# Kernel tuning notes

Hardware: AMD Instinct MI355X
Metric: run time of the kernel (lower is better)

## Reference

```python
import jax, jax.numpy as jnp
import numpy as np

B, S, D = 2, 2048, 1024
H, KV, HD = 16, 4, 64          # heads, kv heads, head_dim = D//H
I, E, K = 3584, 4, 2            # ffn intermediate, routed experts, top_k
WIN = 512                       # sliding window
EPS = 1e-5
THETA = 1000000.0
LIMIT = 7.0                     # swiglu clamp
NREP = H // KV
NEG = -1e30

def _rms(x, w):
    return x * jax.lax.rsqrt(jnp.mean(x * x, axis=-1, keepdims=True) + EPS) * w

def _rot_half(x):
    h = x.shape[-1] // 2
    return jnp.concatenate([-x[..., h:], x[..., :h]], axis=-1)

def _ffn(x, gw, uw, dw):
    g = jnp.minimum(x @ gw.T, LIMIT)
    u = jnp.clip(x @ uw.T, -LIMIT, LIMIT)
    return (jax.nn.silu(g) * u) @ dw.T

def setup_inputs():
    key = jax.random.key(0)
    ks = jax.random.split(key, 16)
    # rotary embeddings [S, HD]
    inv = 1.0 / (THETA ** (jnp.arange(0, HD, 2, dtype=jnp.float32) / HD))
    freqs = jnp.outer(jnp.arange(S, dtype=jnp.float32), inv)
    emb = jnp.concatenate([freqs, freqs], axis=-1)
    s = 0.02
    return dict(
        x=jax.random.normal(ks[0], (B, S, D), jnp.float32),
        cos=jnp.cos(emb), sin=jnp.sin(emb),
        attn_norm_w=jnp.ones((D,), jnp.float32),
        post_norm_w=jnp.ones((D,), jnp.float32),
        q_norm_w=jnp.ones((HD,), jnp.float32),
        k_norm_w=jnp.ones((HD,), jnp.float32),
        wq=jax.random.normal(ks[1], (H * HD, D), jnp.float32) * s,
        wk=jax.random.normal(ks[2], (KV * HD, D), jnp.float32) * s,
        wv=jax.random.normal(ks[3], (KV * HD, D), jnp.float32) * s,
        wo=jax.random.normal(ks[4], (D, H * HD), jnp.float32) * s,
        sinks=jax.random.normal(ks[5], (H,), jnp.float32),
        gate_w=jax.random.normal(ks[6], (E, D), jnp.float32) * s,
        eg_w=jax.random.normal(ks[7], (E, I, D), jnp.float32) * s,
        eu_w=jax.random.normal(ks[8], (E, I, D), jnp.float32) * s,
        ed_w=jax.random.normal(ks[9], (E, D, I), jnp.float32) * s,
        sg_w=jax.random.normal(ks[10], (I, D), jnp.float32) * s,
        su_w=jax.random.normal(ks[11], (I, D), jnp.float32) * s,
        sd_w=jax.random.normal(ks[12], (D, I), jnp.float32) * s,
    )

def _forward(x, cos, sin, attn_norm_w, wq, wk, wv, wo, q_norm_w, k_norm_w,
             sinks, post_norm_w, gate_w, eg_w, eu_w, ed_w, sg_w, su_w, sd_w):
    # ---- attention sublayer ----
    hin = _rms(x, attn_norm_w)
    q = (hin @ wq.T).reshape(B, S, H, HD)
    k = (hin @ wk.T).reshape(B, S, KV, HD)
    v = (hin @ wv.T).reshape(B, S, KV, HD)
    q = _rms(q, q_norm_w)
    k = _rms(k, k_norm_w)
    c, sn = cos[None, :, None, :], sin[None, :, None, :]
    q = q * c + _rot_half(q) * sn
    k = k * c + _rot_half(k) * sn
    k = jnp.repeat(k, NREP, axis=2)  # GQA -> [B,S,H,HD]
    v = jnp.repeat(v, NREP, axis=2)
    scores = jnp.einsum('bihd,bjhd->bhij', q, k) / np.sqrt(HD).astype(np.float32)
    idx = jnp.arange(S)
    allowed = (idx[:, None] >= idx[None, :]) & (idx[None, :] > idx[:, None] - WIN)
    scores = jnp.where(allowed[None, None], scores, NEG)
    sink = jnp.broadcast_to(sinks.reshape(1, H, 1, 1), (B, H, S, 1))
    ext = jnp.concatenate([scores, sink], axis=-1)           # [B,H,S,S+1]
    w = jax.nn.softmax(ext.astype(jnp.float32), axis=-1)[..., :-1].astype(x.dtype)
    attn = jnp.einsum('bhij,bjhd->bihd', w, v).reshape(B, S, H * HD) @ wo.T
    h1 = x + attn
    # ---- MoE FFN sublayer ----
    m = _rms(h1, post_norm_w).reshape(-1, D)                 # [T,D]
    T = m.shape[0]
    gs = jax.nn.softmax(m @ gate_w.T, axis=-1)               # [T,E]
    tw, ti = jax.lax.top_k(gs, K)
    tw = tw / (jnp.sum(tw, axis=-1, keepdims=True) + 1e-20)  # norm_topk_prob
    wd = jnp.zeros((T, E), m.dtype).at[jnp.arange(T)[:, None], ti].add(tw)
    g = jnp.minimum(jnp.einsum('td,eid->tei', m, eg_w), LIMIT)
    u = jnp.clip(jnp.einsum('td,eid->tei', m, eu_w), -LIMIT, LIMIT)
    eo = jnp.einsum('tei,edi->ted', jax.nn.silu(g) * u, ed_w)
    y = jnp.einsum('ted,te->td', eo, wd) + _ffn(m, sg_w, su_w, sd_w)
    return h1 + y.reshape(B, S, D)

def reference(x, cos, sin, attn_norm_w, post_norm_w, q_norm_w, k_norm_w,
              wq, wk, wv, wo, sinks, gate_w, eg_w, eu_w, ed_w, sg_w, su_w, sd_w):
    return _forward(x, cos, sin, attn_norm_w, wq, wk, wv, wo, q_norm_w, k_norm_w,
                    sinks, post_norm_w, gate_w, eg_w, eu_w, ed_w, sg_w, su_w, sd_w)
```

## Files before the change

kernel.cpp:

```cpp
#include <hip/hip_runtime.h>
#include <cstdint>
#include <cstddef>

#define S_LEN 2048
#define BATCH 2
#define DMODEL 1024
#define NH 16
#define NKV 4
#define HDIM 64
#define NTOK 4096
#define IDIM 3584
#define NEXP 4
#define WINSZ 512
#define EPSV 1e-5f
#define LIMV 7.0f
#define CATMAX 13056

typedef unsigned short u16;
typedef unsigned int u32;
typedef __bf16 bf16x8 __attribute__((ext_vector_type(8)));
typedef float f32x4 __attribute__((ext_vector_type(4)));
typedef u32 u32x4 __attribute__((ext_vector_type(4)));
typedef u16 u16x4 __attribute__((ext_vector_type(4)));

__device__ __forceinline__ u16 f2b(float f) {
  union { float f; u32 u; } v; v.f = f;
  return (u16)((v.u + 0x7fffu + ((v.u >> 16) & 1u)) >> 16);
}
__device__ __forceinline__ float b2f(u16 h) {
  union { u32 u; float f; } v; v.u = ((u32)h) << 16; return v.f;
}
__device__ __forceinline__ float wave_sum(float x) {
#pragma unroll
  for (int o = 32; o > 0; o >>= 1) x += __shfl_xor(x, o);
  return x;
}
__device__ __forceinline__ void gld16(const void* g, void* l) {
  __builtin_amdgcn_global_load_lds(
      (const __attribute__((address_space(1))) u32*)g,
      (__attribute__((address_space(3))) u32*)l, 16, 0, 0);
}

__global__ void k_init(int* cnt) {
  if (threadIdx.x < NEXP) cnt[threadIdx.x] = 0;
}

struct CvtArgs {
  const float* src[10];
  u16* dh[10];
  u16* dl[10];
  int n4[10];
};
__global__ __launch_bounds__(256) void k_convert(CvtArgs a) {
  int ai = blockIdx.y;
  const f32x4* s = (const f32x4*)a.src[ai];
  u16* dh = a.dh[ai];
  u16* dl = a.dl[ai];
  int n4 = a.n4[ai];
  for (int i = blockIdx.x * 256 + threadIdx.x; i < n4; i += gridDim.x * 256) {
    f32x4 v = s[i];
    u16x4 h;
    h.x = f2b(v.x); h.y = f2b(v.y); h.z = f2b(v.z); h.w = f2b(v.w);
    ((u16x4*)dh)[i] = h;
    if (dl) {
      u16x4 lo;
      lo.x = f2b(v.x - b2f(h.x)); lo.y = f2b(v.y - b2f(h.y));
      lo.z = f2b(v.z - b2f(h.z)); lo.w = f2b(v.w - b2f(h.w));
      ((u16x4*)dl)[i] = lo;
    }
  }
}

__global__ __launch_bounds__(256) void k_rms_split(const float* __restrict__ x,
                                                   const float* __restrict__ w,
                                                   u16* __restrict__ oh, u16* __restrict__ ol) {
  int row = blockIdx.x;
  int t = threadIdx.x;
  const f32x4* xr = (const f32x4*)(x + (size_t)row * DMODEL);
  f32x4 v = xr[t];
  float ss = v.x * v.x + v.y * v.y + v.z * v.z + v.w * v.w;
  ss = wave_sum(ss);
  __shared__ float red[4];
  int wid = t >> 6;
  if ((t & 63) == 0) red[wid] = ss;
  __syncthreads();
  float tot = red[0] + red[1] + red[2] + red[3];
  float r = rsqrtf(tot * (1.0f / DMODEL) + EPSV);
  f32x4 wv = ((const f32x4*)w)[t];
  float y0 = v.x * r * wv.x, y1 = v.y * r * wv.y, y2 = v.z * r * wv.z, y3 = v.w * r * wv.w;
  u16x4 h; h.x = f2b(y0); h.y = f2b(y1); h.z = f2b(y2); h.w = f2b(y3);
  u16x4 lo; lo.x = f2b(y0 - b2f(h.x)); lo.y = f2b(y1 - b2f(h.y));
  lo.z = f2b(y2 - b2f(h.z)); lo.w = f2b(y3 - b2f(h.w));
  ((u16x4*)(oh + (size_t)row * DMODEL))[t] = h;
  ((u16x4*)(ol + (size_t)row * DMODEL))[t] = lo;
}

__global__ __launch_bounds__(256) void k_qkprep(const float* __restrict__ qkv,
                                                const float* __restrict__ cosb,
                                                const float* __restrict__ sinb,
                                                const float* __restrict__ qw,
                                                const float* __restrict__ kw,
                                                u16* __restrict__ qhh, u16* __restrict__ qll,
                                                u16* __restrict__ khh, u16* __restrict__ kll,
                                                u16* __restrict__ vhh, u16* __restrict__ vll) {
  int t = blockIdx.x;
  int b = t / S_LEN, s = t - b * S_LEN;
  int wid = threadIdx.x >> 6, l = threadIdx.x & 63;
  const float* row = qkv + (size_t)t * 1536;
  float c = cosb[s * 64 + l], sn = sinb[s * 64 + l];
#pragma unroll
  for (int ii = 0; ii < 6; ii++) {
    int u = wid + 4 * ii;
    if (u < 16) {
      float v = row[u * 64 + l];
      float ss = wave_sum(v * v);
      float r = rsqrtf(ss * (1.0f / 64.0f) + EPSV);
      float vn = v * r * qw[l];
      float p = __shfl_xor(vn, 32);
      float o = (l < 32) ? (vn * c - p * sn) : (vn * c + p * sn);
      o *= 0.125f;
      size_t base = (((size_t)(b * NH + u)) * S_LEN + s) * 64 + l;
      u16 hi = f2b(o);
      qhh[base] = hi; qll[base] = f2b(o - b2f(hi));
    } else if (u < 20) {
      int kv = u - 16;
      float v = row[1024 + kv * 64 + l];
      float ss = wave_sum(v * v);
      float r = rsqrtf(ss * (1.0f / 64.0f) + EPSV);
      float vn = v * r * kw[l];
      float p = __shfl_xor(vn, 32);
      float o = (l < 32) ? (vn * c - p * sn) : (vn * c + p * sn);
      size_t base = (((size_t)(b * NKV + kv)) * S_LEN + s) * 64 + l;
      u16 hi = f2b(o);
      khh[base] = hi; kll[base] = f2b(o - b2f(hi));
    } else {
      int kv = u - 20;
      float v = row[1280 + kv * 64 + l];
      size_t base = (((size_t)(b * NKV + kv)) * S_LEN + s) * 64 + l;
      u16 hi = f2b(v);
      vhh[base] = hi; vll[base] = f2b(v - b2f(hi));
    }
  }
}

__global__ __launch_bounds__(256) void k_vtrans(const u16* __restrict__ vh,
                                                const u16* __restrict__ vl,
                                                u16* __restrict__ vth, u16* __restrict__ vtl) {
  int kb = blockIdx.x;
  int gg = blockIdx.y;
  __shared__ u16 Th[128 * 64], Tl[128 * 64];
  int t = threadIdx.x;
  const u16* sh = vh + (((size_t)gg * S_LEN) + kb * 128) * 64;
  const u16* sl = vl + (((size_t)gg * S_LEN) + kb * 128) * 64;
#pragma unroll
  for (int p = 0; p < 8; p++) {
    int idx = p * 256 + t;
    int key = idx >> 4, dq = idx & 15;
    u16x4 a = *(const u16x4*)(sh + key * 64 + dq * 4);
    u16x4 bb = *(const u16x4*)(sl + key * 64 + dq * 4);
    int off = key * 128 + ((dq * 8) ^ ((key & 7) << 4));
    *(u16x4*)((char*)Th + off) = a;
    *(u16x4*)((char*)Tl + off) = bb;
  }
  __syncthreads();
  int d = t >> 2, kq = t & 3;
  u16 outh[32], outl[32];
#pragma unroll
  for (int jj = 0; jj < 32; jj++) {
    int key = kq * 32 + jj;
    int off = key * 128 + ((d * 2) ^ ((key & 7) << 4));
    outh[jj] = *(const u16*)((const char*)Th + off);
    outl[jj] = *(const u16*)((const char*)Tl + off);
  }
  u16* dsth = vth + (((size_t)gg * 64) + d) * S_LEN + kb * 128 + kq * 32;
  u16* dstl = vtl + (((size_t)gg * 64) + d) * S_LEN + kb * 128 + kq * 32;
#pragma unroll
  for (int q4 = 0; q4 < 8; q4++) {
    u16x4 a = {outh[q4 * 4], outh[q4 * 4 + 1], outh[q4 * 4 + 2], outh[q4 * 4 + 3]};
    u16x4 bb = {outl[q4 * 4], outl[q4 * 4 + 1], outl[q4 * 4 + 2], outl[q4 * 4 + 3]};
    *(u16x4*)(dsth + q4 * 4) = a;
    *(u16x4*)(dstl + q4 * 4) = bb;
  }
}

__global__ __launch_bounds__(256) void k_attn_mfma(
    const u16* __restrict__ qhp, const u16* __restrict__ qlp,
    const u16* __restrict__ khp, const u16* __restrict__ klp,
    const u16* __restrict__ vthp, const u16* __restrict__ vtlp,
    const float* __restrict__ sinks,
    u16* __restrict__ oh, u16* __restrict__ ol) {
  int qt = blockIdx.x;
  int bh = blockIdx.y;
  int h = bh & 15, b = bh >> 4;
  int kvg = b * NKV + (h >> 2);
  int qbase = qt * 64;
  int t = threadIdx.x, w = t >> 6, l = t & 63;
  int g = l >> 4, li = l & 15;

  __shared__ u16 Qh[4096], Ql[4096], Kh[4096], Kl[4096], Vh[4096], Vl[4096];
  __shared__ u16 Ph[4][1024], Pl[4][1024];

  {
    const u16* sh = qhp + (((size_t)bh * S_LEN) + qbase) * 64;
    const u16* sl = qlp + (((size_t)bh * S_LEN) + qbase) * 64;
#pragma unroll
    for (int p = 0; p < 2; p++) {
      int idx = p * 256 + t;
      int row = idx >> 3, seg = idx & 7;
      u32x4 a = *(const u32x4*)(sh + row * 64 + seg * 8);
      u32x4 bb = *(const u32x4*)(sl + row * 64 + seg * 8);
      int off = row * 128 + ((seg * 16) ^ ((row & 7) << 4));
      *(u32x4*)((char*)Qh + off) = a;
      *(u32x4*)((char*)Ql + off) = bb;
    }
  }

  float m_[4], lsum[4];
  f32x4 accv[4];
  float sk = sinks[h];
#pragma unroll
  for (int j = 0; j < 4; j++) { m_[j] = sk; lsum[j] = 1.0f; }
#pragma unroll
  for (int nt = 0; nt < 4; nt++) accv[nt] = (f32x4){0.f, 0.f, 0.f, 0.f};

  int j0s = qbase - WINSZ; if (j0s < 0) j0s = 0;
  const u16* khb = khp + ((size_t)kvg * S_LEN) * 64;
  const u16* klb = klp + ((size_t)kvg * S_LEN) * 64;
  const u16* vthb = vthp + ((size_t)kvg * 64) * S_LEN;
  const u16* vtlb = vtlp + ((size_t)kvg * 64) * S_LEN;

  for (int j0 = j0s; j0 <= qbase; j0 += 64) {
    __syncthreads();
#pragma unroll
    for (int p = 0; p < 2; p++) {
      int idx = p * 256 + t;
      int row = idx >> 3, seg = idx & 7;
      int off = row * 128 + ((seg * 16) ^ ((row & 7) << 4));
      *(u32x4*)((char*)Kh + off) = *(const u32x4*)(khb + ((size_t)(j0 + row)) * 64 + seg * 8);
      *(u32x4*)((char*)Kl + off) = *(const u32x4*)(klb + ((size_t)(j0 + row)) * 64 + seg * 8);
      *(u32x4*)((char*)Vh + off) = *(const u32x4*)(vthb + (size_t)row * S_LEN + j0 + seg * 8);
      *(u32x4*)((char*)Vl + off) = *(const u32x4*)(vtlb + (size_t)row * S_LEN + j0 + seg * 8);
    }
    __syncthreads();

    f32x4 S[4];
#pragma unroll
    for (int nt = 0; nt < 4; nt++) S[nt] = (f32x4){0.f, 0.f, 0.f, 0.f};
#pragma unroll
    for (int ks = 0; ks < 2; ks++) {
      int arow = w * 16 + li;
      int coff = ks * 64 + g * 16;
      int ao = arow * 128 + (coff ^ ((arow & 7) << 4));
      bf16x8 qah = *(const bf16x8*)((char*)Qh + ao);
      bf16x8 qal = *(const bf16x8*)((char*)Ql + ao);
#pragma unroll
      for (int nt = 0; nt < 4; nt++) {
        int brow = nt * 16 + li;
        int bo = brow * 128 + (coff ^ ((brow & 7) << 4));
        bf16x8 kbh = *(const bf16x8*)((char*)Kh + bo);
        bf16x8 kbl = *(const bf16x8*)((char*)Kl + bo);
        S[nt] = __builtin_amdgcn_mfma_f32_16x16x32_bf16(qah, kbh, S[nt], 0, 0, 0);
        S[nt] = __builtin_amdgcn_mfma_f32_16x16x32_bf16(qah, kbl, S[nt], 0, 0, 0);
        S[nt] = __builtin_amdgcn_mfma_f32_16x16x32_bf16(qal, kbh, S[nt], 0, 0, 0);
      }
    }

    float scj[4];
#pragma unroll
    for (int j = 0; j < 4; j++) {
      int q = qbase + w * 16 + g * 4 + j;
      float sv[4];
      float mx = -1e30f;
#pragma unroll
      for (int nt = 0; nt < 4; nt++) {
        int key = j0 + nt * 16 + li;
        bool ok = (key <= q) && (key > q - WINSZ);
        sv[nt] = ok ? S[nt][j] : -1e30f;
        mx = fmaxf(mx, sv[nt]);
      }
#pragma unroll
      for (int o = 1; o < 16; o <<= 1) mx = fmaxf(mx, __shfl_xor(mx, o));
      float mn = fmaxf(m_[j], mx);
      float sc = __expf(m_[j] - mn);
      float ps = 0.f;
      float pv[4];
#pragma unroll
      for (int nt = 0; nt < 4; nt++) { pv[nt] = __expf(sv[nt] - mn); ps += pv[nt]; }
#pragma unroll
      for (int o = 1; o < 16; o <<= 1) ps += __shfl_xor(ps, o);
      lsum[j] = lsum[j] * sc + ps;
      m_[j] = mn;
      scj[j] = sc;
      int prow = g * 4 + j;
#pragma unroll
      for (int nt = 0; nt < 4; nt++) {
        int pb = prow * 128 + ((nt * 32 + li * 2) ^ ((prow & 7) << 4));
        u16 hi = f2b(pv[nt]);
        *(u16*)((char*)Ph[w] + pb) = hi;
        *(u16*)((char*)Pl[w] + pb) = f2b(pv[nt] - b2f(hi));
      }
    }
#pragma unroll
    for (int nt = 0; nt < 4; nt++) {
      f32x4 a = accv[nt];
      a[0] *= scj[0]; a[1] *= scj[1]; a[2] *= scj[2]; a[3] *= scj[3];
      accv[nt] = a;
    }

#pragma unroll
    for (int ks = 0; ks < 2; ks++) {
      int coff = ks * 64 + g * 16;
      int pb = li * 128 + (coff ^ ((li & 7) << 4));
      bf16x8 pah = *(const bf16x8*)((char*)Ph[w] + pb);
      bf16x8 pal = *(const bf16x8*)((char*)Pl[w] + pb);
#pragma unroll
      for (int nt = 0; nt < 4; nt++) {
        int vrow = nt * 16 + li;
        int vo = vrow * 128 + (coff ^ ((vrow & 7) << 4));
        bf16x8 vbh = *(const bf16x8*)((char*)Vh + vo);
        bf16x8 vbl = *(const bf16x8*)((char*)Vl + vo);
        accv[nt] = __builtin_amdgcn_mfma_f32_16x16x32_bf16(pah, vbh, accv[nt], 0, 0, 0);
        accv[nt] = __builtin_amdgcn_mfma_f32_16x16x32_bf16(pah, vbl, accv[nt], 0, 0, 0);
        accv[nt] = __builtin_amdgcn_mfma_f32_16x16x32_bf16(pal, vbh, accv[nt], 0, 0, 0);
      }
    }
  }

  float inv[4];
#pragma unroll
  for (int j = 0; j < 4; j++) inv[j] = 1.0f / lsum[j];
#pragma unroll
  for (int nt = 0; nt < 4; nt++) {
#pragma unroll
    for (int j = 0; j < 4; j++) {
      float o = accv[nt][j] * inv[j];
      int token = b * S_LEN + qbase + w * 16 + g * 4 + j;
      size_t off = (size_t)token * (NH * HDIM) + h * 64 + nt * 16 + li;
      u16 hi = f2b(o);
      oh[off] = hi;
      ol[off] = f2b(o - b2f(hi));
    }
  }
}

__global__ __launch_bounds__(256) void k_routing1(const float* __restrict__ h1,
                                                  const float* __restrict__ pw,
                                                  const float* __restrict__ gw,
                                                  u16* __restrict__ mb,
                                                  float* __restrict__ lgbuf) {
  int row = blockIdx.x;
  int t = threadIdx.x;
  int wid = t >> 6;
  const f32x4* xr = (const f32x4*)(h1 + (size_t)row * DMODEL);
  f32x4 v = xr[t];
  float ss = wave_sum(v.x * v.x + v.y * v.y + v.z * v.z + v.w * v.w);
  __shared__ float red[4];
  __shared__ float redp[4][4];
  if ((t & 63) == 0) red[wid] = ss;
  __syncthreads();
  float tot = red[0] + red[1] + red[2] + red[3];
  float r = rsqrtf(tot * (1.0f / DMODEL) + EPSV);
  f32x4 w4 = ((const f32x4*)pw)[t];
  float m0 = v.x * r * w4.x, m1 = v.y * r * w4.y, m2 = v.z * r * w4.z, m3 = v.w * r * w4.w;
  u16x4 hb; hb.x = f2b(m0); hb.y = f2b(m1); hb.z = f2b(m2); hb.w = f2b(m3);
  ((u16x4*)(mb + (size_t)row * DMODEL))[t] = hb;
#pragma unroll
  for (int e = 0; e < NEXP; e++) {
    f32x4 g4 = ((const f32x4*)(gw + (size_t)e * DMODEL))[t];
    float pe = wave_sum(m0 * g4.x + m1 * g4.y + m2 * g4.z + m3 * g4.w);
    if ((t & 63) == 0) redp[wid][e] = pe;
  }
  __syncthreads();
  if (t < NEXP) {
    float lg = redp[0][t] + redp[1][t] + redp[2][t] + redp[3][t];
    lgbuf[(size_t)row * NEXP + t] = lg;
  }
}

__global__ __launch_bounds__(256) void k_route2(const float* __restrict__ lgbuf,
                                                float* __restrict__ wd,
                                                int* __restrict__ cnt,
                                                int* __restrict__ idxb) {
  __shared__ int lcnt[NEXP], gbase[NEXP];
  int t = threadIdx.x;
  int token = blockIdx.x * 256 + t;
  if (t < NEXP) lcnt[t] = 0;
  __syncthreads();
  f32x4 lgv = ((const f32x4*)lgbuf)[token];
  float lg[4] = {lgv.x, lgv.y, lgv.z, lgv.w};
  int i1 = 0;
#pragma unroll
  for (int e = 1; e < NEXP; e++) if (lg[e] > lg[i1]) i1 = e;
  int i2 = -1;
#pragma unroll
  for (int e = 0; e < NEXP; e++) if (e != i1 && (i2 < 0 || lg[e] > lg[i2])) i2 = e;
  float d = __expf(lg[i2] - lg[i1]);
  float w1 = 1.0f / (1.0f + d);
  float w2 = 1.0f - w1;
  float wrow[4] = {0.f, 0.f, 0.f, 0.f};
  wrow[i1] = w1; wrow[i2] = w2;
  ((f32x4*)wd)[token] = (f32x4){wrow[0], wrow[1], wrow[2], wrow[3]};
  int r1 = atomicAdd(&lcnt[i1], 1);
  int r2 = atomicAdd(&lcnt[i2], 1);
  __syncthreads();
  if (t < NEXP) gbase[t] = atomicAdd(&cnt[t], lcnt[t]);
  __syncthreads();
  idxb[i1 * NTOK + gbase[i1] + r1] = token * 2;
  idxb[i2 * NTOK + gbase[i2] + r2] = token * 2 + 1;
}

__global__ __launch_bounds__(256) void k_route3(const int* __restrict__ cnt,
                                                const int* __restrict__ idxb,
                                                const float* __restrict__ wd,
                                                int* __restrict__ idxcat,
                                                float* __restrict__ wcat,
                                                int* __restrict__ pref) {
  int i = blockIdx.x * 256 + threadIdx.x;
  int c0 = cnt[0], c1 = cnt[1], c2 = cnt[2], c3 = cnt[3];
  int p1 = (c0 + 255) & ~255;
  int p2 = p1 + ((c1 + 255) & ~255);
  int p3 = p2 + ((c2 + 255) & ~255);
  int p4 = p3 + ((c3 + 255) & ~255);
  int p5 = p4 + NTOK;
  if (i == 0) {
    pref[0] = 0; pref[1] = p1; pref[2] = p2; pref[3] = p3; pref[4] = p4; pref[5] = p5;
  }
  if (i >= CATMAX) return;
  if (i >= p5) { idxcat[i] = -1; wcat[i] = 0.f; return; }
  if (i >= p4) {
    idxcat[i] = (i - p4) * 4 + 2;
    wcat[i] = 1.0f;
    return;
  }
  int e, base, cn;
  if (i < p1) { e = 0; base = 0; cn = c0; }
  else if (i < p2) { e = 1; base = p1; cn = c1; }
  else if (i < p3) { e = 2; base = p2; cn = c2; }
  else { e = 3; base = p3; cn = c3; }
  int j = i - base;
  if (j < cn) {
    int entry = idxb[e * NTOK + j];
    idxcat[i] = (entry >> 1) * 4 + (entry & 1);
    wcat[i] = wd[(size_t)(entry >> 1) * NEXP + e];
  } else {
    idxcat[i] = -1;
    wcat[i] = 0.f;
  }
}

template <bool DUAL>
__global__ __launch_bounds__(512, 2) void k256(
    const u16* __restrict__ A, const u16* __restrict__ B1e,
    const u16* __restrict__ B2e,
    int lda, int ldb, int K,
    const int* __restrict__ idxcat, const float* __restrict__ wcat,
    const int* __restrict__ pref,
    u16* __restrict__ actout, u16* __restrict__ y3) {
  __shared__ u16 As[2][256 * 64];
  __shared__ u16 Bs[2][128 * 64];
  __shared__ u16 Bus[2][DUAL ? 128 * 64 : 1];
  int tm = blockIdx.y, tn = blockIdx.x;
  int Meff = pref[5];
  int r0 = tm * 256;
  if (r0 >= Meff) return;
  int e = (r0 < pref[1]) ? 0 : (r0 < pref[2]) ? 1 : (r0 < pref[3]) ? 2
          : (r0 < pref[4]) ? 3 : 4;
  const u16* B1 = B1e + (size_t)e * IDIM * DMODEL;
  const u16* B2 = DUAL ? (B2e + (size_t)e * IDIM * DMODEL) : nullptr;

  int t = threadIdx.x;
  int w = t >> 6, l = t & 63;
  int wm = w >> 2, wn = w & 3;
  int li = l & 15, lh = l >> 4;

  size_t aOff[4];
  int seg = t & 7;
#pragma unroll
  for (int c = 0; c < 4; c++) {
    int r = c * 64 + (t >> 3);
    int swz = (seg ^ (r & 7)) * 8;
    int row;
    if constexpr (DUAL) {
      int en = idxcat[r0 + r];
      row = (en >= 0) ? (en >> 2) : 0;
    } else {
      row = r0 + r;
    }
    aOff[c] = (size_t)row * lda + swz;
  }
  size_t bOff[2];
#pragma unroll
  for (int c = 0; c < 2; c++) {
    int r = c * 64 + (t >> 3);
    int swz = (seg ^ (r & 7)) * 8;
    bOff[c] = (size_t)(tn * 128 + r) * ldb + swz;
  }
  int wlds = w * 1024;

  f32x4 acc[8][2];
  f32x4 accU[DUAL ? 8 : 1][2];
#pragma unroll
  for (int f = 0; f < 8; f++)
#pragma unroll
    for (int cf = 0; cf < 2; cf++) {
      acc[f][cf] = (f32x4){0.f, 0.f, 0.f, 0.f};
      if constexpr (DUAL) accU[f][cf] = (f32x4){0.f, 0.f, 0.f, 0.f};
    }

  auto stage = [&](int buf, int k0) {
    char* ab = (char*)As[buf];
#pragma unroll
    for (int c = 0; c < 4; c++) gld16(A + aOff[c] + k0, ab + c * 8192 + wlds);
    char* bb = (char*)Bs[buf];
#pragma unroll
    for (int c = 0; c < 2; c++) gld16(B1 + bOff[c] + k0, bb + c * 8192 + wlds);
    if constexpr (DUAL) {
      char* ub = (char*)Bus[buf];
#pragma unroll
      for (int c = 0; c < 2; c++) gld16(B2 + bOff[c] + k0, ub + c * 8192 + wlds);
    }
  };

  stage(0, 0);
  __syncthreads();

  int NT = K >> 6;
  int cur = 0;
  for (int kt = 0; kt < NT; kt++) {
    if (kt + 1 < NT) stage(cur ^ 1, (kt + 1) << 6);
#pragma unroll
    for (int kk = 0; kk < 2; kk++) {
      bf16x8 af[8];
#pragma unroll
      for (int f = 0; f < 8; f++) {
        int r = wm * 128 + f * 16 + li;
        af[f] = *(const bf16x8*)((const char*)As[cur] + r * 128 +
                                 (((kk * 4 + lh) ^ (r & 7)) << 4));
      }
      bf16x8 bfr[2];
#pragma unroll
      for (int cf = 0; cf < 2; cf++) {
        int r = wn * 32 + cf * 16 + li;
        bfr[cf] = *(const bf16x8*)((const char*)Bs[cur] + r * 128 +
                                   (((kk * 4 + lh) ^ (r & 7)) << 4));
      }
#pragma unroll
      for (int f = 0; f < 8; f++)
#pragma unroll
        for (int cf = 0; cf < 2; cf++)
          acc[f][cf] = __builtin_amdgcn_mfma_f32_16x16x32_bf16(af[f], bfr[cf], acc[f][cf], 0, 0, 0);
      if constexpr (DUAL) {
        bf16x8 bu[2];
#pragma unroll
        for (int cf = 0; cf < 2; cf++) {
          int r = wn * 32 + cf * 16 + li;
          bu[cf] = *(const bf16x8*)((const char*)Bus[cur] + r * 128 +
                                    (((kk * 4 + lh) ^ (r & 7)) << 4));
        }
#pragma unroll
        for (int f = 0; f < 8; f++)
#pragma unroll
          for (int cf = 0; cf < 2; cf++)
            accU[f][cf] = __builtin_amdgcn_mfma_f32_16x16x32_bf16(af[f], bu[cf], accU[f][cf], 0, 0, 0);
      }
    }
    __syncthreads();
    cur ^= 1;
  }

#pragma unroll
  for (int f = 0; f < 8; f++) {
#pragma unroll
    for (int j = 0; j < 4; j++) {
      int r = r0 + wm * 128 + f * 16 + lh * 4 + j;
#pragma unroll
      for (int cf = 0; cf < 2; cf++) {
        int c = tn * 128 + wn * 32 + cf * 16 + li;
        if constexpr (DUAL) {
          float g = acc[f][cf][j];
          float u = accU[f][cf][j];
          float gm = fminf(g, LIMV);
          float um = fminf(fmaxf(u, -LIMV), LIMV);
          float a = gm / (1.0f + __expf(-gm)) * um;
          actout[(size_t)r * IDIM + c] = f2b(a);
        } else {
          int entry = idxcat[r];
          if (entry >= 0) {
            int tok = entry >> 2, slot = entry & 3;
            y3[((size_t)slot * NTOK + tok) * DMODEL + c] = f2b(wcat[r] * acc[f][cf][j]);
          }
        }
      }
    }
  }
}

constexpr int EPI_STORE = 0;
constexpr int EPI_H1 = 1;

template <int EPI>
__global__ __launch_bounds__(256, 2) void k_gemm(
    const u16* __restrict__ Ah, const u16* __restrict__ Al,
    const u16* __restrict__ Bh, const u16* __restrict__ Bl,
    int M, int N, int K, int lda, int ldb,
    float* __restrict__ outF, int ldc, int col0,
    const float* __restrict__ addsrc) {
  __shared__ u16 As[2 * 128 * 32];
  __shared__ u16 Bs[2 * 128 * 32];
  int tm = blockIdx.y, tn = blockIdx.x;
  int t = threadIdx.x;
  int w = t >> 6, l = t & 63;
  int wr = w >> 1, wc = w & 1;

  size_t a0 = (size_t)(tm * 128 + (t >> 2)) * lda + (t & 3) * 8;
  size_t a1 = a0 + (size_t)64 * lda;
  size_t b0 = (size_t)(tn * 128 + (t >> 2)) * ldb + (t & 3) * 8;
  size_t b1 = b0 + (size_t)64 * ldb;

  char* AsW0 = (char*)As + w * 1024;
  char* AsW1 = (char*)As + 4096 + w * 1024;
  char* BsW0 = (char*)Bs + w * 1024;
  char* BsW1 = (char*)Bs + 4096 + w * 1024;

  f32x4 acc[4][4];
#pragma unroll
  for (int i = 0; i < 4; i++)
#pragma unroll
    for (int j = 0; j < 4; j++) acc[i][j] = (f32x4){0.f, 0.f, 0.f, 0.f};

  int arow = wr * 64 + (l & 15);
  int brow = wc * 64 + (l & 15);
  int koff = (l >> 4) * 8;

  for (int k0 = 0; k0 < K; k0 += 32) {
    __syncthreads();
    gld16(Ah + a0 + k0, AsW0);
    gld16(Ah + a1 + k0, AsW1);
    gld16(Bh + b0 + k0, BsW0);
    gld16(Bh + b1 + k0, BsW1);
    gld16(Al + a0 + k0, AsW0 + 8192);
    gld16(Al + a1 + k0, AsW1 + 8192);
    gld16(Bl + b0 + k0, BsW0 + 8192);
    gld16(Bl + b1 + k0, BsW1 + 8192);
    __syncthreads();
    bf16x8 af[2][4], bf[2][4];
#pragma unroll
    for (int mm = 0; mm < 4; mm++) {
      af[0][mm] = *(const bf16x8*)&As[(arow + mm * 16) * 32 + koff];
      bf[0][mm] = *(const bf16x8*)&Bs[(brow + mm * 16) * 32 + koff];
      af[1][mm] = *(const bf16x8*)&As[128 * 32 + (arow + mm * 16) * 32 + koff];
      bf[1][mm] = *(const bf16x8*)&Bs[128 * 32 + (brow + mm * 16) * 32 + koff];
    }
#pragma unroll
    for (int mi = 0; mi < 4; mi++)
#pragma unroll
      for (int ni = 0; ni < 4; ni++) {
        acc[mi][ni] = __builtin_amdgcn_mfma_f32_16x16x32_bf16(af[0][mi], bf[0][ni], acc[mi][ni], 0, 0, 0);
        acc[mi][ni] = __builtin_amdgcn_mfma_f32_16x16x32_bf16(af[0][mi], bf[1][ni], acc[mi][ni], 0, 0, 0);
        acc[mi][ni] = __builtin_amdgcn_mfma_f32_16x16x32_bf16(af[1][mi], bf[0][ni], acc[mi][ni], 0, 0, 0);
      }
  }

  int rb = tm * 128 + wr * 64 + ((l >> 4) << 2);
  int cb = tn * 128 + wc * 64 + (l & 15);
#pragma unroll
  for (int mi = 0; mi < 4; mi++) {
#pragma unroll
    for (int j = 0; j < 4; j++) {
      int r = rb + mi * 16 + j;
#pragma unroll
      for (int ni = 0; ni < 4; ni++) {
        int c = cb + ni * 16;
        float v = acc[mi][ni][j];
        if constexpr (EPI == EPI_STORE) {
          outF[(size_t)r * ldc + col0 + c] = v;
        } else {
          size_t o = (size_t)r * ldc + c;
          outF[o] = v + addsrc[o];
        }
      }
    }
  }
}

__global__ __launch_bounds__(256) void k_final(const float* __restrict__ h1,
                                               const u16* __restrict__ y3,
                                               float* __restrict__ out) {
  int i = blockIdx.x * 256 + threadIdx.x;
  f32x4 a = ((const f32x4*)h1)[i];
  u16x4 s0 = ((const u16x4*)y3)[i];
  u16x4 s1 = ((const u16x4*)(y3 + (size_t)NTOK * DMODEL))[i];
  u16x4 s2 = ((const u16x4*)(y3 + (size_t)2 * NTOK * DMODEL))[i];
  f32x4 r = {a.x + b2f(s0.x) + b2f(s1.x) + b2f(s2.x),
             a.y + b2f(s0.y) + b2f(s1.y) + b2f(s2.y),
             a.z + b2f(s0.z) + b2f(s1.z) + b2f(s2.z),
             a.w + b2f(s0.w) + b2f(s1.w) + b2f(s2.w)};
  ((f32x4*)out)[i] = r;
}

extern "C" void kernel_launch(void* const* d_in, const int* in_sizes, int n_in,
                              void* d_out, int out_size, void* d_ws, size_t ws_size,
                              hipStream_t stream) {
  (void)in_sizes; (void)n_in; (void)out_size; (void)ws_size;
  const float* x = (const float*)d_in[0];
  const float* cosb = (const float*)d_in[1];
  const float* sinb = (const float*)d_in[2];
  const float* anw = (const float*)d_in[3];
  const float* pnw = (const float*)d_in[4];
  const float* qnw = (const float*)d_in[5];
  const float* knw = (const float*)d_in[6];
  const float* wq = (const float*)d_in[7];
  const float* wk = (const float*)d_in[8];
  const float* wv = (const float*)d_in[9];
  const float* wo = (const float*)d_in[10];
  const float* sinks = (const float*)d_in[11];
  const float* gw = (const float*)d_in[12];
  const float* egw = (const float*)d_in[13];
  const float* euw = (const float*)d_in[14];
  const float* edw = (const float*)d_in[15];
  const float* sgw = (const float*)d_in[16];
  const float* suw = (const float*)d_in[17];
  const float* sdw = (const float*)d_in[18];
  float* out = (float*)d_out;

  char* ws = (char*)d_ws;
  size_t off = 0;
  auto alloc = [&](size_t bytes) -> char* {
    char* p = ws + off;
    off += (bytes + 255) & ~(size_t)255;
    return p;
  };
  const size_t EW = (size_t)IDIM * DMODEL;
  u16* wqkvh = (u16*)alloc((size_t)1536 * 1024 * 2);
  u16* wqkvl = (u16*)alloc((size_t)1536 * 1024 * 2);
  u16* woh = (u16*)alloc(1048576 * 2); u16* wol = (u16*)alloc(1048576 * 2);
  u16* egb5 = (u16*)alloc(5 * EW * 2);
  u16* eub5 = (u16*)alloc(5 * EW * 2);
  u16* edb5 = (u16*)alloc(5 * EW * 2);
  float* h1 = (float*)alloc((size_t)NTOK * DMODEL * 4);
  u16* mb = (u16*)alloc((size_t)NTOK * DMODEL * 2);
  u16* y3 = (u16*)alloc((size_t)3 * NTOK * DMODEL * 2);
  float* wdbuf = (float*)alloc((size_t)NTOK * NEXP * 4);
  float* lgbuf = (float*)alloc((size_t)NTOK * NEXP * 4);
  int* cnt = (int*)alloc(256);
  int* idxb = (int*)alloc((size_t)NEXP * NTOK * 4);
  int* idxcat = (int*)alloc((size_t)CATMAX * 4);
  float* wcat = (float*)alloc((size_t)CATMAX * 4);
  int* pref = (int*)alloc(256);
  char* regA = alloc((size_t)CATMAX * IDIM * 2);
  float* qkvb = (float*)regA;
  u16* qh_ = (u16*)(regA + 25165824);
  u16* ql_ = (u16*)(regA + 33554432);
  u16* kh_ = (u16*)(regA + 41943040);
  u16* kl_ = (u16*)(regA + 44040192);
  u16* vh_ = (u16*)(regA + 46137344);
  u16* vl_ = (u16*)(regA + 48234496);
  u16* vth_ = (u16*)(regA + 50331648);
  u16* vtl_ = (u16*)(regA + 52428800);
  u16* hinh = (u16*)(regA + 54525952);
  u16* hinl = (u16*)(regA + 62914560);
  u16* attnh = (u16*)(regA + 71303168);
  u16* attnl = (u16*)(regA + 79691776);
  u16* actcat = (u16*)regA;

  k_init<<<1, 64, 0, stream>>>(cnt);

  CvtArgs ca;
  const float* srcs[10] = {wq, wk, wv, wo, egw, euw, edw, sgw, suw, sdw};
  u16* dhs[10] = {wqkvh, wqkvh + 1048576, wqkvh + 1310720, woh,
                  egb5, eub5, edb5, egb5 + 4 * EW, eub5 + 4 * EW, edb5 + 4 * EW};
  u16* dls[10] = {wqkvl, wqkvl + 1048576, wqkvl + 1310720, wol,
                  nullptr, nullptr, nullptr, nullptr, nullptr, nullptr};
  int ns[10] = {1048576, 262144, 262144, 1048576, 14680064, 14680064, 14680064,
                3670016, 3670016, 3670016};
  for (int i = 0; i < 10; i++) {
    ca.src[i] = srcs[i]; ca.dh[i] = dhs[i]; ca.dl[i] = dls[i]; ca.n4[i] = ns[i] / 4;
  }
  k_convert<<<dim3(2048, 10), 256, 0, stream>>>(ca);

  k_rms_split<<<NTOK, 256, 0, stream>>>(x, anw, hinh, hinl);

  k_gemm<EPI_STORE><<<dim3(12, 32), 256, 0, stream>>>(
      hinh, hinl, wqkvh, wqkvl, NTOK, 1536, 1024, 1024, 1024,
      qkvb, 1536, 0, nullptr);

  k_qkprep<<<NTOK, 256, 0, stream>>>(qkvb, cosb, sinb, qnw, knw,
                                     qh_, ql_, kh_, kl_, vh_, vl_);
  k_vtrans<<<dim3(16, 8), 256, 0, stream>>>(vh_, vl_, vth_, vtl_);
  k_attn_mfma<<<dim3(32, 32), 256, 0, stream>>>(qh_, ql_, kh_, kl_, vth_, vtl_,
                                                sinks, attnh, attnl);

  k_gemm<EPI_H1><<<dim3(8, 32), 256, 0, stream>>>(
      attnh, attnl, woh, wol, NTOK, 1024, 1024, 1024, 1024,
      h1, 1024, 0, x);

  k_routing1<<<NTOK, 256, 0, stream>>>(h1, pnw, gw, mb, lgbuf);
  k_route2<<<16, 256, 0, stream>>>(lgbuf, wdbuf, cnt, idxb);
  k_route3<<<CATMAX / 256, 256, 0, stream>>>(cnt, idxb, wdbuf, idxcat, wcat, pref);

  k256<true><<<dim3(IDIM / 128, CATMAX / 256), 512, 0, stream>>>(
      mb, egb5, eub5, DMODEL, DMODEL, DMODEL, idxcat, wcat, pref, actcat, nullptr);
  k256<false><<<dim3(DMODEL / 128, CATMAX / 256), 512, 0, stream>>>(
      actcat, edb5, nullptr, IDIM, IDIM, IDIM, idxcat, wcat, pref, nullptr, y3);

  k_final<<<4096, 256, 0, stream>>>(h1, y3, out);
}
```

Baseline: 688.9 us.

## Split MoE GEMM into gate-up and down kernels with XCD-aware block swizzle

Splits the templated MoE GEMM into two dedicated kernels. Both remap block IDs so that neighbouring tiles land on the same XCD, which should improve L2 reuse of expert weights. The down-projection kernel now uses a 32-wide K tile with a new LDS layout and launch bounds of 4 blocks per CU, aiming for higher occupancy and less LDS per block. The trade-off is more K iterations and more barriers in the down projection, plus heavier index arithmetic to address the new layout.

```diff
diff --git a/kernel.cpp b/kernel.cpp
--- a/kernel.cpp
+++ b/kernel.cpp
@@ -39,6 +39,11 @@
   __builtin_amdgcn_global_load_lds(
       (const __attribute__((address_space(1))) u32*)g,
       (__attribute__((address_space(3))) u32*)l, 16, 0, 0);
+}
+__device__ __forceinline__ int xcd_swz(int id, int nwg) {
+  int q = nwg >> 3, rr = nwg & 7;
+  int xcd = id & 7, j = id >> 3;
+  return (xcd < rr ? xcd * (q + 1) : rr * (q + 1) + (xcd - rr) * q) + j;
 }
 
 __global__ void k_init(int* cnt) {
@@ -448,25 +453,24 @@
   }
 }
 
-template <bool DUAL>
-__global__ __launch_bounds__(512, 2) void k256(
+__global__ __launch_bounds__(512, 2) void k256gu(
     const u16* __restrict__ A, const u16* __restrict__ B1e,
     const u16* __restrict__ B2e,
-    int lda, int ldb, int K,
-    const int* __restrict__ idxcat, const float* __restrict__ wcat,
-    const int* __restrict__ pref,
-    u16* __restrict__ actout, u16* __restrict__ y3) {
+    const int* __restrict__ idxcat, const int* __restrict__ pref,
+    u16* __restrict__ actout) {
   __shared__ u16 As[2][256 * 64];
   __shared__ u16 Bs[2][128 * 64];
-  __shared__ u16 Bus[2][DUAL ? 128 * 64 : 1];
-  int tm = blockIdx.y, tn = blockIdx.x;
+  __shared__ u16 Bus[2][128 * 64];
+  int nwg = gridDim.x * gridDim.y;
+  int swzid = xcd_swz(blockIdx.y * gridDim.x + blockIdx.x, nwg);
+  int tn = swzid % gridDim.x, tm = swzid / gridDim.x;
   int Meff = pref[5];
   int r0 = tm * 256;
   if (r0 >= Meff) return;
   int e = (r0 < pref[1]) ? 0 : (r0 < pref[2]) ? 1 : (r0 < pref[3]) ? 2
           : (r0 < pref[4]) ? 3 : 4;
   const u16* B1 = B1e + (size_t)e * IDIM * DMODEL;
-  const u16* B2 = DUAL ? (B2e + (size_t)e * IDIM * DMODEL) : nullptr;
+  const u16* B2 = B2e + (size_t)e * IDIM * DMODEL;
 
   int t = threadIdx.x;
   int w = t >> 6, l = t & 63;
@@ -479,32 +483,26 @@
   for (int c = 0; c < 4; c++) {
     int r = c * 64 + (t >> 3);
     int swz = (seg ^ (r & 7)) * 8;
-    int row;
-    if constexpr (DUAL) {
-      int en = idxcat[r0 + r];
-      row = (en >= 0) ? (en >> 2) : 0;
-    } else {
-      row = r0 + r;
-    }
-    aOff[c] = (size_t)row * lda + swz;
+    int en = idxcat[r0 + r];
+    int row = (en >= 0) ? (en >> 2) : 0;
+    aOff[c] = (size_t)row * DMODEL + swz;
   }
   size_t bOff[2];
 #pragma unroll
   for (int c = 0; c < 2; c++) {
     int r = c * 64 + (t >> 3);
     int swz = (seg ^ (r & 7)) * 8;
-    bOff[c] = (size_t)(tn * 128 + r) * ldb + swz;
+    bOff[c] = (size_t)(tn * 128 + r) * DMODEL + swz;
   }
   int wlds = w * 1024;
 
-  f32x4 acc[8][2];
-  f32x4 accU[DUAL ? 8 : 1][2];
+  f32x4 acc[8][2], accU[8][2];
 #pragma unroll
   for (int f = 0; f < 8; f++)
 #pragma unroll
     for (int cf = 0; cf < 2; cf++) {
       acc[f][cf] = (f32x4){0.f, 0.f, 0.f, 0.f};
-      if constexpr (DUAL) accU[f][cf] = (f32x4){0.f, 0.f, 0.f, 0.f};
+      accU[f][cf] = (f32x4){0.f, 0.f, 0.f, 0.f};
     }
 
   auto stage = [&](int buf, int k0) {
@@ -514,17 +512,15 @@
     char* bb = (char*)Bs[buf];
 #pragma unroll
     for (int c = 0; c < 2; c++) gld16(B1 + bOff[c] + k0, bb + c * 8192 + wlds);
-    if constexpr (DUAL) {
-      char* ub = (char*)Bus[buf];
-#pragma unroll
-      for (int c = 0; c < 2; c++) gld16(B2 + bOff[c] + k0, ub + c * 8192 + wlds);
-    }
+    char* ub = (char*)Bus[buf];
+#pragma unroll
+    for (int c = 0; c < 2; c++) gld16(B2 + bOff[c] + k0, ub + c * 8192 + wlds);
   };
 
   stage(0, 0);
   __syncthreads();
 
-  int NT = K >> 6;
+  int NT = DMODEL >> 6;
   int cur = 0;
   for (int kt = 0; kt < NT; kt++) {
     if (kt + 1 < NT) stage(cur ^ 1, (kt + 1) << 6);
@@ -549,20 +545,18 @@
 #pragma unroll
         for (int cf = 0; cf < 2; cf++)
           acc[f][cf] = __builtin_amdgcn_mfma_f32_16x16x32_bf16(af[f], bfr[cf], acc[f][cf], 0, 0, 0);
-      if constexpr (DUAL) {
-        bf16x8 bu[2];
-#pragma unroll
-        for (int cf = 0; cf < 2; cf++) {
-          int r = wn * 32 + cf * 16 + li;
-          bu[cf] = *(const bf16x8*)((const char*)Bus[cur] + r * 128 +
-                                    (((kk * 4 + lh) ^ (r & 7)) << 4));
-        }
-#pragma unroll
-        for (int f = 0; f < 8; f++)
-#pragma unroll
-          for (int cf = 0; cf < 2; cf++)
-            accU[f][cf] = __builtin_amdgcn_mfma_f32_16x16x32_bf16(af[f], bu[cf], accU[f][cf], 0, 0, 0);
-      }
+      bf16x8 bu[2];
+#pragma unroll
+      for (int cf = 0; cf < 2; cf++) {
+        int r = wn * 32 + cf * 16 + li;
+        bu[cf] = *(const bf16x8*)((const char*)Bus[cur] + r * 128 +
+                                  (((kk * 4 + lh) ^ (r & 7)) << 4));
+      }
+#pragma unroll
+      for (int f = 0; f < 8; f++)
+#pragma unroll
+        for (int cf = 0; cf < 2; cf++)
+          accU[f][cf] = __builtin_amdgcn_mfma_f32_16x16x32_bf16(af[f], bu[cf], accU[f][cf], 0, 0, 0);
     }
     __syncthreads();
     cur ^= 1;
@@ -576,19 +570,106 @@
 #pragma unroll
       for (int cf = 0; cf < 2; cf++) {
         int c = tn * 128 + wn * 32 + cf * 16 + li;
-        if constexpr (DUAL) {
-          float g = acc[f][cf][j];
-          float u = accU[f][cf][j];
-          float gm = fminf(g, LIMV);
-          float um = fminf(fmaxf(u, -LIMV), LIMV);
-          float a = gm / (1.0f + __expf(-gm)) * um;
-          actout[(size_t)r * IDIM + c] = f2b(a);
-        } else {
-          int entry = idxcat[r];
-          if (entry >= 0) {
-            int tok = entry >> 2, slot = entry & 3;
-            y3[((size_t)slot * NTOK + tok) * DMODEL + c] = f2b(wcat[r] * acc[f][cf][j]);
-          }
+        float g = acc[f][cf][j];
+        float u = accU[f][cf][j];
+        float gm = fminf(g, LIMV);
+        float um = fminf(fmaxf(u, -LIMV), LIMV);
+        float a = gm / (1.0f + __expf(-gm)) * um;
+        actout[(size_t)r * IDIM + c] = f2b(a);
+      }
+    }
+  }
+}
+
+__global__ __launch_bounds__(512, 4) void k256d(
+    const u16* __restrict__ A, const u16* __restrict__ B1e,
+    const int* __restrict__ idxcat, const float* __restrict__ wcat,
+    const int* __restrict__ pref,
+    u16* __restrict__ y3) {
+  __shared__ u16 As[2][256 * 32];
+  __shared__ u16 B1s[2][128 * 32];
+  int nwg = gridDim.x * gridDim.y;
+  int swzid = xcd_swz(blockIdx.y * gridDim.x + blockIdx.x, nwg);
+  int tn = swzid % gridDim.x, tm = swzid / gridDim.x;
+  int Meff = pref[5];
+  int r0 = tm * 256;
+  if (r0 >= Meff) return;
+  int e = (r0 < pref[1]) ? 0 : (r0 < pref[2]) ? 1 : (r0 < pref[3]) ? 2
+          : (r0 < pref[4]) ? 3 : 4;
+  const u16* B1 = B1e + (size_t)e * DMODEL * IDIM;
+
+  int t = threadIdx.x;
+  int w = t >> 6, l = t & 63;
+  int wm = w >> 2, wn = w & 3;
+  int li = l & 15, lh = l >> 4;
+
+  int g = (l & 7) ^ (l >> 3);
+  int kchunk = g & 3;
+  size_t aG[2];
+#pragma unroll
+  for (int c = 0; c < 2; c++) {
+    int rA = c * 64 + w * 8 + (l >> 3) + 128 * (g >> 2);
+    aG[c] = (size_t)(r0 + rA) * IDIM + kchunk * 8;
+  }
+  size_t bG;
+  {
+    int rB = w * 8 + (l >> 3) + 64 * (g >> 2);
+    bG = (size_t)(tn * 128 + rB) * IDIM + kchunk * 8;
+  }
+  int wlds = w * 1024;
+
+  int abase = li * 128 + (((wm * 4 + lh) ^ (li & 7)) << 4);
+  int bbase = ((wn & 1) * 32 + li) * 128 + ((((wn >> 1) * 4 + lh) ^ (li & 7)) << 4);
+
+  f32x4 acc[8][2];
+#pragma unroll
+  for (int f = 0; f < 8; f++)
+#pragma unroll
+    for (int cf = 0; cf < 2; cf++) acc[f][cf] = (f32x4){0.f, 0.f, 0.f, 0.f};
+
+  auto stage = [&](int buf, int k0) {
+    char* as = (char*)As[buf];
+    gld16(A + aG[0] + k0, as + wlds);
+    gld16(A + aG[1] + k0, as + 8192 + wlds);
+    gld16(B1 + bG + k0, (char*)B1s[buf] + wlds);
+  };
+
+  stage(0, 0);
+  __syncthreads();
+
+  int NT = IDIM >> 5;
+  int cur = 0;
+  for (int kt = 0; kt < NT; kt++) {
+    if (kt + 1 < NT) stage(cur ^ 1, (kt + 1) << 5);
+    bf16x8 af[8];
+#pragma unroll
+    for (int f = 0; f < 8; f++)
+      af[f] = *(const bf16x8*)((const char*)As[cur] + abase + f * 2048);
+    bf16x8 b1f[2];
+#pragma unroll
+    for (int cf = 0; cf < 2; cf++)
+      b1f[cf] = *(const bf16x8*)((const char*)B1s[cur] + bbase + cf * 2048);
+#pragma unroll
+    for (int f = 0; f < 8; f++)
+#pragma unroll
+      for (int cf = 0; cf < 2; cf++)
+        acc[f][cf] = __builtin_amdgcn_mfma_f32_16x16x32_bf16(af[f], b1f[cf], acc[f][cf], 0, 0, 0);
+    __syncthreads();
+    cur ^= 1;
+  }
+
+#pragma unroll
+  for (int f = 0; f < 8; f++) {
+#pragma unroll
+    for (int j = 0; j < 4; j++) {
+      int r = r0 + wm * 128 + f * 16 + lh * 4 + j;
+#pragma unroll
+      for (int cf = 0; cf < 2; cf++) {
+        int c = tn * 128 + wn * 32 + cf * 16 + li;
+        int entry = idxcat[r];
+        if (entry >= 0) {
+          int tok = entry >> 2, slot = entry & 3;
+          y3[((size_t)slot * NTOK + tok) * DMODEL + c] = f2b(wcat[r] * acc[f][cf][j]);
         }
       }
     }
@@ -798,10 +879,10 @@
   k_route2<<<16, 256, 0, stream>>>(lgbuf, wdbuf, cnt, idxb);
   k_route3<<<CATMAX / 256, 256, 0, stream>>>(cnt, idxb, wdbuf, idxcat, wcat, pref);
 
-  k256<true><<<dim3(IDIM / 128, CATMAX / 256), 512, 0, stream>>>(
-      mb, egb5, eub5, DMODEL, DMODEL, DMODEL, idxcat, wcat, pref, actcat, nullptr);
-  k256<false><<<dim3(DMODEL / 128, CATMAX / 256), 512, 0, stream>>>(
-      actcat, edb5, nullptr, IDIM, IDIM, IDIM, idxcat, wcat, pref, nullptr, y3);
+  k256gu<<<dim3(IDIM / 128, CATMAX / 256), 512, 0, stream>>>(
+      mb, egb5, eub5, idxcat, pref, actcat);
+  k256d<<<dim3(DMODEL / 128, CATMAX / 256), 512, 0, stream>>>(
+      actcat, edb5, idxcat, wcat, pref, y3);
 
   k_final<<<4096, 256, 0, stream>>>(h1, y3, out);
 }
```

Measured after the change: 617.4 us, median of 2. -10.4%, faster.
